# Optimization experiments

Measured on AMD Instinct MI355X. Metric: run time of the kernel, lower is better.

Reference implementation:

```python
import jax, jax.numpy as jnp
import numpy as np

HEADS = 8
DIM_HEAD = 64
EPS = 1e-5  # fp32 eps in ChanLayerNorm


def chan_layer_norm(x, g):
    # x: [b, c, h, w]; normalize over channel dim with biased variance
    mean = jnp.mean(x, axis=1, keepdims=True)
    var = jnp.var(x, axis=1, keepdims=True)
    return (x - mean) * jax.lax.rsqrt(var + EPS) * g[None, :, None, None]


def setup_inputs() -> dict:
    key = jax.random.key(0)
    k1, k2, k3 = jax.random.split(key, 3)
    dim, inner = 512, HEADS * DIM_HEAD
    fmap = jax.random.normal(k1, (16, dim, 64, 64), dtype=jnp.float32)
    # 1x1 conv weights (no bias); scaled like typical init to keep softmax unsaturated
    w_qkv = jax.random.normal(k2, (3 * inner, dim), dtype=jnp.float32) * 0.02
    w_out = jax.random.normal(k3, (dim, inner), dtype=jnp.float32) * 0.02
    g1 = jnp.ones((dim,), dtype=jnp.float32)
    g2 = jnp.ones((dim,), dtype=jnp.float32)
    return {"fmap": fmap, "g1": g1, "w_qkv": w_qkv, "w_out": w_out, "g2": g2}


def reference(fmap, g1, w_qkv, w_out, g2):
    b, c, X, Y = fmap.shape
    h, dh = HEADS, DIM_HEAD
    n = X * Y  # seq_len
    scale = dh ** -0.5

    x = chan_layer_norm(fmap, g1)
    # 1x1 conv == channel matmul: [b, 3*inner, X, Y]
    qkv = jnp.einsum('bcxy,oc->boxy', x, w_qkv)
    q, k, v = jnp.split(qkv, 3, axis=1)

    def to_bhnc(t):
        # b (h c) x y -> b h n c
        return t.reshape(b, h, dh, n).transpose(0, 1, 3, 2)

    q, k, v = map(to_bhnc, (q, k, v))

    q = jax.nn.softmax(q, axis=-1) * scale          # softmax over feature dim
    k = jax.nn.softmax(k, axis=2)                   # softmax over seq dim
    v = v / jnp.linalg.norm(v, axis=-1, keepdims=True)  # l2norm
    inv_sqrt_n = 1.0 / np.sqrt(n)
    k = k * inv_sqrt_n
    v = v * inv_sqrt_n

    context = jnp.einsum('bhnd,bhne->bhde', k, v)   # small d x e context
    out = jnp.einsum('bhnd,bhde->bhne', q, context)  # [b, h, n, dh]

    # b h n d -> b (h d) x y
    out = out.transpose(0, 1, 3, 2).reshape(b, h * dh, X, Y)
    out = jax.nn.gelu(out, approximate=False)
    out = jnp.einsum('bcxy,oc->boxy', out, w_out)
    return chan_layer_norm(out, g2)
```

## Files before the change

### kernel.cpp

```cpp
#include <hip/hip_runtime.h>

typedef unsigned short u16;
typedef __attribute__((ext_vector_type(2))) float f32x2;
typedef __attribute__((ext_vector_type(4))) float f32x4;
typedef __attribute__((ext_vector_type(8))) short s16x8;
typedef __attribute__((ext_vector_type(8))) u16 u16x8;
typedef __attribute__((ext_vector_type(4))) u16 u16x4;

#define NB 16
#define CD 512
#define NS 4096
#define NHD 8

#define SBAR  __builtin_amdgcn_s_barrier()
#define SCHED __builtin_amdgcn_sched_barrier(0)
#define LGKM0 asm volatile("s_waitcnt lgkmcnt(0)" ::: "memory")
#define PRIO1 __builtin_amdgcn_s_setprio(1)
#define PRIO0 __builtin_amdgcn_s_setprio(0)

__device__ __forceinline__ float bf2f(u16 u){
  union { unsigned int i; float f; } z; z.i = ((unsigned int)u) << 16; return z.f;
}
__device__ __forceinline__ u16 f2bf(float f){
  union { float f; unsigned int i; } z; z.f = f;
  unsigned int i = z.i;
  return (u16)((i + 0x7fffu + ((i >> 16) & 1u)) >> 16);
}
__device__ __forceinline__ float gelu_f(float x){
  return 0.5f * x * (1.0f + erff(x * 0.70710678118654752440f));
}
__device__ __forceinline__ void gl_lds16(const u16* g, u16* l){
  __builtin_amdgcn_global_load_lds((const __attribute__((address_space(1))) void*)(g),
                                   (__attribute__((address_space(3))) void*)(l), 16, 0, 0);
}

__global__ void prep_w_k(const float* __restrict__ wqkv, const float* __restrict__ g1,
                         const float* __restrict__ wout, u16* __restrict__ w1b,
                         u16* __restrict__ w2b){
  int i = blockIdx.x * 256 + threadIdx.x;
  if (i < 1536*512) {
    w1b[i] = f2bf(wqkv[i] * g1[i & 511]);
  } else {
    int j = i - 1536*512;
    w2b[j] = f2bf(wout[j]);
  }
}

__global__ __launch_bounds__(512) void ln1t_k(const float* __restrict__ fmap,
                                              u16* __restrict__ xlnT){
  int b = blockIdx.y, n0 = blockIdx.x * 32;
  int t = threadIdx.x;
  int lane = t & 63, wv = t >> 6;
  __shared__ u16 Lb[512][40];
  __shared__ u16 Tt[64][36];
  __shared__ float red1[8][8][4], red2[8][8][4];
  __shared__ float mean_s[32], rstd_s[32];

  int ng = t & 7;
  float s1[4] = {0,0,0,0}, s2[4] = {0,0,0,0};
  const float* fb = fmap + ((size_t)b*CD)*NS + n0 + ng*4;
  #pragma unroll
  for (int it = 0; it < 8; ++it){
    int q = it*512 + t;
    int c = q >> 3;
    f32x4 v = *(const f32x4*)&fb[(size_t)c*NS];
    u16x4 pk;
    #pragma unroll
    for (int j = 0; j < 4; ++j){
      pk[j] = f2bf(v[j]);
      s1[j] += v[j]; s2[j] += v[j]*v[j];
    }
    *(u16x4*)&Lb[c][ng*4] = pk;
  }
  #pragma unroll
  for (int off = 8; off < 64; off <<= 1)
    #pragma unroll
    for (int j = 0; j < 4; ++j){
      s1[j] += __shfl_xor(s1[j], off, 64);
      s2[j] += __shfl_xor(s2[j], off, 64);
    }
  if (lane < 8){
    #pragma unroll
    for (int j = 0; j < 4; ++j){ red1[wv][lane][j] = s1[j]; red2[wv][lane][j] = s2[j]; }
  }
  __syncthreads();
  if (t < 32){
    int g = t >> 2, j = t & 3;
    float a = 0.f, bq = 0.f;
    #pragma unroll
    for (int w = 0; w < 8; ++w){ a += red1[w][g][j]; bq += red2[w][g][j]; }
    float mn = a * (1.f/512.f);
    float var = bq * (1.f/512.f) - mn*mn;
    mean_s[t] = mn; rstd_s[t] = rsqrtf(var + 1e-5f);
  }
  __syncthreads();

  for (int ct = 0; ct < 8; ++ct){
    {
      int cl = t >> 3, n4 = (t & 7) * 4;
      u16x4 xv = *(const u16x4*)&Lb[ct*64 + cl][n4];
      u16x4 pk;
      #pragma unroll
      for (int j = 0; j < 4; ++j)
        pk[j] = f2bf((bf2f(xv[j]) - mean_s[n4+j]) * rstd_s[n4+j]);
      *(u16x4*)&Tt[cl][n4] = pk;
    }
    __syncthreads();
    {
      int nr = t >> 4, c4 = t & 15;
      u16x4 w;
      #pragma unroll
      for (int j = 0; j < 4; ++j) w[j] = Tt[c4*4 + j][nr];
      *(u16x4*)&xlnT[((size_t)b*NS + n0 + nr)*CD + ct*64 + c4*4] = w;
    }
    __syncthreads();
  }
}

__global__ __launch_bounds__(512) void gemm1_k(const u16* __restrict__ A,
                                               const u16* __restrict__ Bm,
                                               u16* __restrict__ Cm){
  __shared__ u16 lds[2][4][8192];
  int bi = blockIdx.x;
  int xcd = bi & 7, r2 = bi >> 3;
  int gi = r2 / 6, yy = r2 - gi*6;
  int g  = gi*8 + xcd;
  int x  = g & 15, z = g >> 4;
  int o0 = yy*256, bn0 = x*256;
  int t = threadIdx.x;
  int lane = t & 63, wv = t >> 6;
  int wm = wv >> 2, wn = wv & 3;
  int fr = lane & 15, fg = lane >> 4;
  const u16* Ab = A + (size_t)o0*512;
  const u16* Bb = Bm + ((size_t)z*NS + bn0)*512;
  int li8 = lane >> 3, scn = lane & 7;

  f32x4 acc[8][4];
  #pragma unroll
  for (int i=0;i<8;++i)
    #pragma unroll
    for (int j=0;j<4;++j) acc[i][j] = (f32x4){0.f,0.f,0.f,0.f};
  s16x8 afr[4][2];
  s16x8 bfr[2][2][2];

  auto stH = [&](int slot, int half, int kt){
    #pragma unroll
    for (int it=0; it<2; ++it){
      int li = it*64 + wv*8 + li8;
      int q  = scn ^ (li & 7);
      int row;
      if (half < 2) row = ((li>>6)<<7) + half*64 + (li & 63);
      else          row = ((li>>5)<<6) + (half-2)*32 + (li & 31);
      const u16* G = (half < 2) ? Ab : Bb;
      gl_lds16(G + (size_t)row*512 + kt + q*8, &lds[slot][half][it*4096 + wv*512]);
    }
  };
  auto ldA = [&](int slot, int mq){
    #pragma unroll
    for (int mr=0;mr<4;++mr)
      #pragma unroll
      for (int ks=0;ks<2;++ks){
        int li = wm*64 + mr*16 + fr;
        int c8 = (ks*4+fg) ^ (li & 7);
        afr[mr][ks] = *(const s16x8*)&lds[slot][mq][li*64 + c8*8];
      }
  };
  auto ldB = [&](int slot, int nq){
    #pragma unroll
    for (int nr=0;nr<2;++nr)
      #pragma unroll
      for (int ks=0;ks<2;++ks){
        int li = wn*32 + nr*16 + fr;
        int c8 = (ks*4+fg) ^ (li & 7);
        bfr[nq][nr][ks] = *(const s16x8*)&lds[slot][2+nq][li*64 + c8*8];
      }
  };
  auto mm = [&](int mq, int nq){
    #pragma unroll
    for (int mr=0;mr<4;++mr)
      #pragma unroll
      for (int nr=0;nr<2;++nr)
        #pragma unroll
        for (int ks=0;ks<2;++ks)
          acc[mq*4+mr][nq*2+nr] = __builtin_amdgcn_mfma_f32_16x16x32_bf16(
              afr[mr][ks], bfr[nq][nr][ks], acc[mq*4+mr][nq*2+nr], 0,0,0);
  };

  stH(0,0,0); stH(0,2,0); stH(0,3,0); stH(0,1,0);
  asm volatile("s_waitcnt vmcnt(2)" ::: "memory");
  SBAR; SCHED;

  #pragma unroll
  for (int kt=0; kt<8; ++kt){
    int slot = kt & 1, ns = slot ^ 1, kn = (kt+1)*64;
    bool F = kt < 7;
    ldA(slot,0); ldB(slot,0); ldB(slot,1);
    if (F){ stH(ns,0,kn); stH(ns,2,kn); stH(ns,3,kn); }
    PRIO1; mm(0,0); mm(0,1); PRIO0;
    if (F) asm volatile("s_waitcnt vmcnt(6)" ::: "memory");
    else   asm volatile("s_waitcnt vmcnt(0)" ::: "memory");
    SBAR; SCHED;
    ldA(slot,1);
    if (F) stH(ns,1,kn);
    PRIO1; mm(1,1); mm(1,0); PRIO0;
    if (F) asm volatile("s_waitcnt vmcnt(2)" ::: "memory");
    SBAR; SCHED;
  }

  size_t cb = (size_t)z * 1536 * NS;
  #pragma unroll
  for (int mq=0;mq<2;++mq)
    #pragma unroll
    for (int mr=0;mr<4;++mr)
      #pragma unroll
      for (int nq=0;nq<2;++nq)
        #pragma unroll
        for (int nr=0;nr<2;++nr){
          int row = o0 + wm*128 + mq*64 + mr*16 + fg*4;
          int col = bn0 + wn*64 + nq*32 + nr*16 + fr;
          #pragma unroll
          for (int r=0;r<4;++r)
            Cm[cb + (size_t)(row+r)*NS + col] = f2bf(acc[mq*4+mr][nq*2+nr][r]);
        }
}

__global__ __launch_bounds__(512, 2) void gemm2ln_k(const u16* __restrict__ A,
                                                    const u16* __restrict__ Bm,
                                                    const float* __restrict__ g2,
                                                    float* __restrict__ out){
  __shared__ u16 lds[2][20480];
  int x = blockIdx.x, z = blockIdx.y;
  int n0 = x*128;
  int t = threadIdx.x;
  int lane = t & 63, wv = t >> 6;
  int wm = wv >> 1, wn = wv & 1;
  int fr = lane & 15, fg = lane >> 4;
  const u16* Ab = A;
  const u16* Bb = Bm + ((size_t)z*NS + n0)*512;

  int l8  = lane >> 3;
  int c8d = lane & 7;

  f32x4 acc[8][4];
  #pragma unroll
  for (int i=0;i<8;++i)
    #pragma unroll
    for (int j=0;j<4;++j) acc[i][j] = (f32x4){0.f,0.f,0.f,0.f};
  s16x8 afr[4], bfr[4];

  auto stA = [&](int slot, int kt, int bt){
    int L  = bt*64 + wv*8 + l8;
    int q  = c8d ^ (l8 & 7);
    int r  = (q >> 2)*256 + L;
    int col = kt + (q & 3)*8;
    gl_lds16(Ab + (size_t)r*512 + col, &lds[slot][(bt*64 + wv*8)*64]);
  };
  auto stB = [&](int slot, int kt){
    int L  = wv*8 + l8;
    int q  = c8d ^ (l8 & 7);
    int r  = (q >> 2)*64 + L;
    int col = kt + (q & 3)*8;
    gl_lds16(Bb + (size_t)r*512 + col, &lds[slot][16384 + (wv*8)*64]);
  };
  auto ldA = [&](int slot, int h){
    #pragma unroll
    for (int mi=0;mi<4;++mi){
      int R = wm*128 + (h*4+mi)*16 + fr;
      int L = R & 255, half = R >> 8;
      int c8 = (half*4 + fg) ^ (L & 7);
      afr[mi] = *(const s16x8*)&lds[slot][L*64 + c8*8];
    }
  };
  auto ldB = [&](int slot){
    #pragma unroll
    for (int nj=0;nj<4;++nj){
      int R = wn*64 + nj*16 + fr;
      int L = R & 63, half = R >> 6;
      int c8 = (half*4 + fg) ^ (L & 7);
      bfr[nj] = *(const s16x8*)&lds[slot][16384 + L*64 + c8*8];
    }
  };
  auto mm16 = [&](int h){
    #pragma unroll
    for (int mi=0;mi<4;++mi)
      #pragma unroll
      for (int nj=0;nj<4;++nj)
        acc[h*4+mi][nj] = __builtin_amdgcn_mfma_f32_16x16x32_bf16(
            afr[mi], bfr[nj], acc[h*4+mi][nj], 0,0,0);
  };

  stA(0,0,0); stA(0,0,1); stB(0,0); stA(0,0,2); stA(0,0,3);
  asm volatile("s_waitcnt vmcnt(0)" ::: "memory");
  SBAR; SCHED;

  #pragma unroll
  for (int kt=0; kt<16; ++kt){
    int slot = kt & 1, ns = slot ^ 1, kn = (kt+1)*32;
    ldA(slot,0); ldB(slot);
    if (kt<15){
      stA(ns,kn,0); stA(ns,kn,1); stB(ns,kn); stA(ns,kn,2); stA(ns,kn,3);
    }
    PRIO1; mm16(0); PRIO0;
    ldA(slot,1);
    PRIO1; mm16(1); PRIO0;
    if (kt<15) asm volatile("s_waitcnt vmcnt(0)" ::: "memory");
    SBAR; SCHED;
  }

  __syncthreads();
  float* red1 = (float*)&lds[0][0];
  float* red2 = red1 + 512;
  float* ms   = red2 + 512;
  float* rs   = ms + 128;
  float s1[4], s2[4];
  #pragma unroll
  for (int nj=0;nj<4;++nj){
    float a = 0.f, b2 = 0.f;
    #pragma unroll
    for (int mi=0;mi<8;++mi)
      #pragma unroll
      for (int r=0;r<4;++r){ float v = acc[mi][nj][r]; a += v; b2 += v*v; }
    s1[nj] = a; s2[nj] = b2;
  }
  #pragma unroll
  for (int off=16; off<64; off<<=1)
    #pragma unroll
    for (int nj=0;nj<4;++nj){
      s1[nj] += __shfl_xor(s1[nj], off, 64);
      s2[nj] += __shfl_xor(s2[nj], off, 64);
    }
  if (fg == 0){
    #pragma unroll
    for (int nj=0;nj<4;++nj){
      int c = wn*64 + nj*16 + fr;
      red1[wm*128 + c] = s1[nj];
      red2[wm*128 + c] = s2[nj];
    }
  }
  __syncthreads();
  if (t < 128){
    float a  = red1[t] + red1[128+t] + red1[256+t] + red1[384+t];
    float b2 = red2[t] + red2[128+t] + red2[256+t] + red2[384+t];
    float mn = a * (1.f/512.f);
    float var = b2 * (1.f/512.f) - mn*mn;
    ms[t] = mn; rs[t] = rsqrtf(var + 1e-5f);
  }
  __syncthreads();
  float mc[4], rc[4];
  #pragma unroll
  for (int nj=0;nj<4;++nj){
    int c = wn*64 + nj*16 + fr;
    mc[nj] = ms[c]; rc[nj] = rs[c];
  }
  float* ob = out + (size_t)z*CD*NS + n0;
  #pragma unroll
  for (int mi=0;mi<8;++mi)
    #pragma unroll
    for (int r=0;r<4;++r){
      int row = wm*128 + mi*16 + fg*4 + r;
      float gg = g2[row];
      #pragma unroll
      for (int nj=0;nj<4;++nj)
        ob[(size_t)row*NS + wn*64 + nj*16 + fr] = (acc[mi][nj][r] - mc[nj])*rc[nj]*gg;
    }
}

__global__ __launch_bounds__(256) void ctxpart_k(const u16* __restrict__ qkv,
                                                 float* __restrict__ part,
                                                 float* __restrict__ mS){
  int chunk = blockIdx.x, bh = blockIdx.y;
  int b = bh >> 3, h = bh & 7;
  int t = threadIdx.x;
  int lane = t & 63, wv = t >> 6;
  int fr = lane & 15, fg = lane >> 4;
  __shared__ u16 KT[64*128];
  __shared__ u16 VT[64*128];
  __shared__ float invn_s[128];
  const u16* kb = qkv + ((size_t)(b*1536 + 512  + h*64))*NS;
  const u16* vb = qkv + ((size_t)(b*1536 + 1024 + h*64))*NS;
  int d = t >> 2, q = t & 3;

  float sloc = 0.f;

  f32x4 acc[4][4];
  #pragma unroll
  for (int i=0;i<4;++i)
    #pragma unroll
    for (int j=0;j<4;++j) acc[i][j] = (f32x4){0.f,0.f,0.f,0.f};

  for (int nt = 0; nt < 4; ++nt){
    int n0 = chunk*512 + nt*128;
    if (nt) __syncthreads();
    u16x8 kreg[4];
    #pragma unroll
    for (int s = 0; s < 4; ++s){
      int c0 = q*32 + s*8;
      u16x8 vv = *(const u16x8*)&vb[(size_t)d*NS + n0 + c0];
      *(u16x8*)&VT[d*128 + (c0 ^ ((d&7)<<3))] = vv;
      kreg[s] = *(const u16x8*)&kb[(size_t)d*NS + n0 + c0];
    }
    __syncthreads();
    {
      int col = t >> 1, half = t & 1;
      float ss = 0.f;
      #pragma unroll
      for (int e2 = 0; e2 < 32; ++e2){
        int e = half*32 + e2;
        float xv = bf2f(VT[e*128 + (col ^ ((e&7)<<3))]);
        ss += xv*xv;
      }
      ss += __shfl_xor(ss, 1, 64);
      if (half == 0) invn_s[col] = rsqrtf(ss);
    }
    __syncthreads();
    #pragma unroll
    for (int s = 0; s < 4; ++s){
      int c0 = q*32 + s*8;
      u16x8 kk = kreg[s];
      u16x8 ek;
      #pragma unroll
      for (int j = 0; j < 8; ++j){
        float e = __expf(bf2f(kk[j]));
        sloc += e;
        ek[j] = f2bf(e * invn_s[c0 + j]);
      }
      *(u16x8*)&KT[d*128 + (c0 ^ ((d&7)<<3))] = ek;
    }
    __syncthreads();
    int kc = wv*32 + fg*8;
    s16x8 af[4], bfr[4];
    #pragma unroll
    for (int i=0;i<4;++i){
      int ra = i*16 + fr;
      af[i]  = *(const s16x8*)&KT[ra*128 + (kc ^ ((ra&7)<<3))];
      bfr[i] = *(const s16x8*)&VT[ra*128 + (kc ^ ((ra&7)<<3))];
    }
    #pragma unroll
    for (int i=0;i<4;++i)
      #pragma unroll
      for (int j=0;j<4;++j)
        acc[i][j] = __builtin_amdgcn_mfma_f32_16x16x32_bf16(af[i], bfr[j], acc[i][j], 0,0,0);
  }

  sloc += __shfl_xor(sloc, 1, 64);
  sloc += __shfl_xor(sloc, 2, 64);
  if (q == 0){
    size_t mb = ((size_t)bh*8 + chunk)*128;
    mS[mb + d]      = 0.0f;
    mS[mb + 64 + d] = sloc;
  }

  float* buf0 = (float*)KT;
  float* buf1 = (float*)VT;
  auto dump = [&](float* bf){
    #pragma unroll
    for (int i=0;i<4;++i)
      #pragma unroll
      for (int j=0;j<4;++j)
        #pragma unroll
        for (int r=0;r<4;++r) bf[((i*4+j)*4+r)*64 + lane] = acc[i][j][r];
  };
  auto addin = [&](float* bf){
    #pragma unroll
    for (int i=0;i<4;++i)
      #pragma unroll
      for (int j=0;j<4;++j)
        #pragma unroll
        for (int r=0;r<4;++r) acc[i][j][r] += bf[((i*4+j)*4+r)*64 + lane];
  };
  __syncthreads();
  if (wv==1) dump(buf0);
  if (wv==3) dump(buf1);
  __syncthreads();
  if (wv==0) addin(buf0);
  if (wv==2) addin(buf1);
  __syncthreads();
  if (wv==2) dump(buf0);
  __syncthreads();
  if (wv==0){
    addin(buf0);
    float* pp = part + ((size_t)bh*8 + chunk)*4096;
    #pragma unroll
    for (int i=0;i<4;++i)
      #pragma unroll
      for (int j=0;j<4;++j)
        #pragma unroll
        for (int r=0;r<4;++r)
          pp[(i*16+fg*4+r)*64 + j*16+fr] = acc[i][j][r];
  }
}

__global__ void ctxred_k(const float* __restrict__ part, const float* __restrict__ mS,
                         float* __restrict__ ctx){
  int bh = blockIdx.x, t = threadIdx.x;
  __shared__ float fs[8][64];
  if (t < 64){
    int d = t;
    float mc[8];
    float mx = -3.0e38f;
    #pragma unroll
    for (int c=0;c<8;++c){ mc[c] = mS[((size_t)bh*8 + c)*128 + d]; mx = fmaxf(mx, mc[c]); }
    float es[8]; float denom = 0.f;
    #pragma unroll
    for (int c=0;c<8;++c){
      es[c] = __expf(mc[c] - mx);
      denom += es[c] * mS[((size_t)bh*8 + c)*128 + 64 + d];
    }
    float inv = 1.0f / (denom * 4096.0f);
    #pragma unroll
    for (int c=0;c<8;++c) fs[c][d] = es[c] * inv;
  }
  __syncthreads();
  #pragma unroll
  for (int i=0;i<16;++i){
    int idx = t + i*256;
    int d = idx >> 6;
    float s = 0.f;
    #pragma unroll
    for (int ch=0; ch<8; ++ch) s += fs[ch][d] * part[((size_t)bh*8 + ch)*4096 + idx];
    ctx[(size_t)bh*4096 + idx] = s;
  }
}

__global__ __launch_bounds__(256) void attnout_k(const u16* __restrict__ qkv,
                                                 const float* __restrict__ ctx,
                                                 u16* __restrict__ gT){
  int bh = blockIdx.y;
  int b = bh >> 3, h = bh & 7;
  int n0 = blockIdx.x * 256;
  int t = threadIdx.x;
  int lane = t & 63, wv = t >> 6;
  int fr = lane & 15, fg = lane >> 4;
  __shared__ u16 P[256][72];
  __shared__ u16 cT[64][72];

  const float* cs = ctx + (size_t)bh*4096;
  #pragma unroll
  for (int i=0;i<16;++i){
    int idx = i*256 + t;
    int d = idx >> 6, e = idx & 63;
    cT[e][d] = f2bf(cs[idx]);
  }

  const u16* qb = qkv + ((size_t)(b*1536 + h*64))*NS + n0 + t;
  float p[64];
  #pragma unroll
  for (int d=0; d<64; ++d) p[d] = bf2f(qb[(size_t)d*NS]);
  float m = p[0];
  #pragma unroll
  for (int d=1; d<64; ++d) m = fmaxf(m, p[d]);
  float s = 0.f;
  #pragma unroll
  for (int d=0; d<64; ++d){ p[d] = __expf(p[d]-m); s += p[d]; }
  float inv = 0.125f / s;
  #pragma unroll
  for (int d0=0; d0<8; ++d0){
    u16x8 pk;
    #pragma unroll
    for (int j=0;j<8;++j) pk[j] = f2bf(p[d0*8+j] * inv);
    *(u16x8*)&P[t][d0*8] = pk;
  }
  __syncthreads();

  f32x4 acc[4][4];
  #pragma unroll
  for (int i=0;i<4;++i)
    #pragma unroll
    for (int j=0;j<4;++j) acc[i][j] = (f32x4){0.f,0.f,0.f,0.f};
  #pragma unroll
  for (int k=0; k<2; ++k){
    s16x8 af[4], bfr[4];
    #pragma unroll
    for (int i=0;i<4;++i){
      af[i]  = *(const s16x8*)&P[wv*64 + i*16 + fr][k*32 + fg*8];
      bfr[i] = *(const s16x8*)&cT[i*16 + fr][k*32 + fg*8];
    }
    #pragma unroll
    for (int i=0;i<4;++i)
      #pragma unroll
      for (int j=0;j<4;++j)
        acc[i][j] = __builtin_amdgcn_mfma_f32_16x16x32_bf16(af[i], bfr[j], acc[i][j], 0,0,0);
  }

  #pragma unroll
  for (int i=0;i<4;++i)
    #pragma unroll
    for (int j=0;j<4;++j)
      #pragma unroll
      for (int r=0;r<4;++r)
        P[wv*64 + i*16 + fg*4 + r][j*16 + fr] = f2bf(gelu_f(acc[i][j][r]));

  int sub = lane >> 4, e4 = (lane & 15) * 4;
  #pragma unroll
  for (int it=0; it<16; ++it){
    int row = wv*64 + it*4 + sub;
    *(u16x4*)&gT[((size_t)b*NS + n0 + row)*CD + h*64 + e4] = *(u16x4*)&P[row][e4];
  }
}

extern "C" void kernel_launch(void* const* d_in, const int* in_sizes, int n_in,
                              void* d_out, int out_size, void* d_ws, size_t ws_size,
                              hipStream_t stream) {
  const float* fmap = (const float*)d_in[0];
  const float* g1   = (const float*)d_in[1];
  const float* wqkv = (const float*)d_in[2];
  const float* wout = (const float*)d_in[3];
  const float* g2   = (const float*)d_in[4];
  float* out = (float*)d_out;

  char* ws = (char*)d_ws;
  size_t off = 0;
  auto alloc = [&](size_t bytes) -> void* {
    void* p = ws + off;
    off += (bytes + 255) & ~(size_t)255;
    return p;
  };
  u16*   qkv  = (u16*)alloc((size_t)16*1536*4096*2);
  u16*   xlnT = (u16*)alloc((size_t)16*4096*512*2);
  u16*   gT   = xlnT;
  float* part = (float*)alloc((size_t)128*8*4096*4);
  float* mS   = (float*)alloc((size_t)128*8*128*4);
  float* ctx  = (float*)alloc((size_t)128*4096*4);
  u16*   w1b  = (u16*)alloc((size_t)1536*512*2);
  u16*   w2b  = (u16*)alloc((size_t)512*512*2);
  if (off > ws_size) return;

  prep_w_k<<<4096, 256, 0, stream>>>(wqkv, g1, wout, w1b, w2b);
  ln1t_k<<<dim3(128,16), 512, 0, stream>>>(fmap, xlnT);
  gemm1_k<<<1536, 512, 0, stream>>>(w1b, xlnT, qkv);
  ctxpart_k<<<dim3(8,128), 256, 0, stream>>>(qkv, part, mS);
  ctxred_k<<<128, 256, 0, stream>>>(part, mS, ctx);
  attnout_k<<<dim3(16,128), 256, 0, stream>>>(qkv, ctx, gT);
  gemm2ln_k<<<dim3(32,16), 512, 0, stream>>>(w2b, gT, g2, out);
}
```

Measured before the change: 314.4 us.

## Fuse attention output and GELU into the output-projection GEMM

The separate attnout kernel is removed. Its work (q softmax over the feature dim, multiply by context, GELU) is now computed per head inside the gemm2 kernel, which writes the GELU tile straight into the swizzled B LDS buffer instead of making a gT round trip through global memory. This saves the bf16 gT write and re-read and one launch. In exchange the GEMM main loop now holds serial softmax and context MFMA phases, uses more LDS, and drops the occupancy hint of 2 from launch_bounds, which may lower occupancy and weaken load overlap.

New measurement: 308.9 us. About the same (-1.8%).

```diff
diff --git a/kernel.cpp b/kernel.cpp
--- a/kernel.cpp
+++ b/kernel.cpp
@@ -14,7 +14,6 @@
 
 #define SBAR  __builtin_amdgcn_s_barrier()
 #define SCHED __builtin_amdgcn_sched_barrier(0)
-#define LGKM0 asm volatile("s_waitcnt lgkmcnt(0)" ::: "memory")
 #define PRIO1 __builtin_amdgcn_s_setprio(1)
 #define PRIO0 __builtin_amdgcn_s_setprio(0)
 
@@ -224,22 +223,25 @@
         }
 }
 
-__global__ __launch_bounds__(512, 2) void gemm2ln_k(const u16* __restrict__ A,
-                                                    const u16* __restrict__ Bm,
-                                                    const float* __restrict__ g2,
-                                                    float* __restrict__ out){
-  __shared__ u16 lds[2][20480];
+__global__ __launch_bounds__(512) void gemm2f_k(const u16* __restrict__ A,
+                                                const u16* __restrict__ qkv,
+                                                const float* __restrict__ ctx,
+                                                const float* __restrict__ g2,
+                                                float* __restrict__ out){
+  __shared__ u16 Ar[2][16384];
+  __shared__ u16 Bh[2][4096];
+  __shared__ u16 P[128][72];
+  __shared__ u16 cT[64][72];
+  __shared__ float invP[128];
   int x = blockIdx.x, z = blockIdx.y;
   int n0 = x*128;
   int t = threadIdx.x;
   int lane = t & 63, wv = t >> 6;
   int wm = wv >> 1, wn = wv & 1;
+  int wn2 = wv >> 2, we = wv & 3;
   int fr = lane & 15, fg = lane >> 4;
+  int l8 = lane >> 3, c8d = lane & 7;
   const u16* Ab = A;
-  const u16* Bb = Bm + ((size_t)z*NS + n0)*512;
-
-  int l8  = lane >> 3;
-  int c8d = lane & 7;
 
   f32x4 acc[8][4];
   #pragma unroll
@@ -248,67 +250,122 @@
     for (int j=0;j<4;++j) acc[i][j] = (f32x4){0.f,0.f,0.f,0.f};
   s16x8 afr[4], bfr[4];
 
-  auto stA = [&](int slot, int kt, int bt){
-    int L  = bt*64 + wv*8 + l8;
-    int q  = c8d ^ (l8 & 7);
-    int r  = (q >> 2)*256 + L;
-    int col = kt + (q & 3)*8;
-    gl_lds16(Ab + (size_t)r*512 + col, &lds[slot][(bt*64 + wv*8)*64]);
-  };
-  auto stB = [&](int slot, int kt){
-    int L  = wv*8 + l8;
-    int q  = c8d ^ (l8 & 7);
-    int r  = (q >> 2)*64 + L;
-    int col = kt + (q & 3)*8;
-    gl_lds16(Bb + (size_t)r*512 + col, &lds[slot][16384 + (wv*8)*64]);
-  };
-  auto ldA = [&](int slot, int h){
+  auto stA4 = [&](int slot, int kt){
+    #pragma unroll
+    for (int bt=0; bt<4; ++bt){
+      int L  = bt*64 + wv*8 + l8;
+      int q  = c8d ^ (l8 & 7);
+      int r  = (q >> 2)*256 + L;
+      int col = kt + (q & 3)*8;
+      gl_lds16(Ab + (size_t)r*512 + col, &Ar[slot][(bt*64 + wv*8)*64]);
+    }
+  };
+  auto ldA = [&](int slot, int h2){
     #pragma unroll
     for (int mi=0;mi<4;++mi){
-      int R = wm*128 + (h*4+mi)*16 + fr;
+      int R = wm*128 + (h2*4+mi)*16 + fr;
       int L = R & 255, half = R >> 8;
       int c8 = (half*4 + fg) ^ (L & 7);
-      afr[mi] = *(const s16x8*)&lds[slot][L*64 + c8*8];
-    }
-  };
-  auto ldB = [&](int slot){
+      afr[mi] = *(const s16x8*)&Ar[slot][L*64 + c8*8];
+    }
+  };
+  auto ldBh = [&](int kt2){
     #pragma unroll
     for (int nj=0;nj<4;++nj){
       int R = wn*64 + nj*16 + fr;
       int L = R & 63, half = R >> 6;
       int c8 = (half*4 + fg) ^ (L & 7);
-      bfr[nj] = *(const s16x8*)&lds[slot][16384 + L*64 + c8*8];
-    }
-  };
-  auto mm16 = [&](int h){
+      bfr[nj] = *(const s16x8*)&Bh[kt2][L*64 + c8*8];
+    }
+  };
+  auto mm16 = [&](int h2){
     #pragma unroll
     for (int mi=0;mi<4;++mi)
       #pragma unroll
       for (int nj=0;nj<4;++nj)
-        acc[h*4+mi][nj] = __builtin_amdgcn_mfma_f32_16x16x32_bf16(
-            afr[mi], bfr[nj], acc[h*4+mi][nj], 0,0,0);
-  };
-
-  stA(0,0,0); stA(0,0,1); stB(0,0); stA(0,0,2); stA(0,0,3);
-  asm volatile("s_waitcnt vmcnt(0)" ::: "memory");
-  SBAR; SCHED;
-
-  #pragma unroll
-  for (int kt=0; kt<16; ++kt){
-    int slot = kt & 1, ns = slot ^ 1, kn = (kt+1)*32;
-    ldA(slot,0); ldB(slot);
-    if (kt<15){
-      stA(ns,kn,0); stA(ns,kn,1); stB(ns,kn); stA(ns,kn,2); stA(ns,kn,3);
-    }
+        acc[h2*4+mi][nj] = __builtin_amdgcn_mfma_f32_16x16x32_bf16(
+            afr[mi], bfr[nj], acc[h2*4+mi][nj], 0,0,0);
+  };
+
+  stA4(0, 0);
+
+  for (int h = 0; h < 8; ++h){
+    const float* cs = ctx + ((size_t)(z*8 + h))*4096;
+    #pragma unroll
+    for (int i=0;i<8;++i){
+      int idx = i*512 + t;
+      cT[idx & 63][idx >> 6] = f2bf(cs[idx]);
+    }
+    {
+      int nl = wv*16 + (lane & 15);
+      int dg = lane >> 4;
+      const u16* qb = qkv + ((size_t)(z*1536 + h*64 + dg*16))*NS + n0 + nl;
+      float p[16];
+      float m = -3.0e38f;
+      #pragma unroll
+      for (int j=0;j<16;++j){ p[j] = bf2f(qb[(size_t)j*NS]); m = fmaxf(m, p[j]); }
+      m = fmaxf(m, __shfl_xor(m, 16, 64));
+      m = fmaxf(m, __shfl_xor(m, 32, 64));
+      float s = 0.f;
+      #pragma unroll
+      for (int j=0;j<16;++j){ p[j] = __expf(p[j]-m); s += p[j]; }
+      s += __shfl_xor(s, 16, 64);
+      s += __shfl_xor(s, 32, 64);
+      u16x8 pk;
+      #pragma unroll
+      for (int j=0;j<8;++j) pk[j] = f2bf(p[j]);
+      *(u16x8*)&P[nl][dg*16] = pk;
+      #pragma unroll
+      for (int j=0;j<8;++j) pk[j] = f2bf(p[8+j]);
+      *(u16x8*)&P[nl][dg*16+8] = pk;
+      if (dg == 0) invP[nl] = 0.125f / s;
+    }
+    __syncthreads();
+    stA4(1, (2*h+1)*32);
+
+    f32x4 a2[4];
+    #pragma unroll
+    for (int i=0;i<4;++i) a2[i] = (f32x4){0.f,0.f,0.f,0.f};
+    #pragma unroll
+    for (int ks=0; ks<2; ++ks){
+      s16x8 bfx = *(const s16x8*)&cT[we*16 + fr][ks*32 + fg*8];
+      #pragma unroll
+      for (int nf=0; nf<4; ++nf){
+        s16x8 afx = *(const s16x8*)&P[wn2*64 + nf*16 + fr][ks*32 + fg*8];
+        a2[nf] = __builtin_amdgcn_mfma_f32_16x16x32_bf16(afx, bfx, a2[nf], 0,0,0);
+      }
+    }
+    {
+      int kt2w = we >> 1;
+      #pragma unroll
+      for (int nf=0; nf<4; ++nf)
+        #pragma unroll
+        for (int r=0; r<4; ++r){
+          int nl2 = wn2*64 + nf*16 + fg*4 + r;
+          int e = we*16 + fr;
+          int col = e & 31;
+          int L = nl2 & 63;
+          int c8 = ((nl2>>6)*4 + (col>>3)) ^ (L & 7);
+          Bh[kt2w][L*64 + c8*8 + (col&7)] = f2bf(gelu_f(a2[nf][r] * invP[nl2]));
+        }
+    }
+    asm volatile("s_waitcnt vmcnt(4)" ::: "memory");
+    __syncthreads();
+    ldA(0,0); ldBh(0);
     PRIO1; mm16(0); PRIO0;
-    ldA(slot,1);
+    ldA(0,1);
     PRIO1; mm16(1); PRIO0;
-    if (kt<15) asm volatile("s_waitcnt vmcnt(0)" ::: "memory");
-    SBAR; SCHED;
-  }
-
-  __syncthreads();
-  float* red1 = (float*)&lds[0][0];
+    asm volatile("s_waitcnt vmcnt(0)" ::: "memory");
+    __syncthreads();
+    if (h < 7) stA4(0, (2*h+2)*32);
+    ldA(1,0); ldBh(1);
+    PRIO1; mm16(0); PRIO0;
+    ldA(1,1);
+    PRIO1; mm16(1); PRIO0;
+  }
+
+  __syncthreads();
+  float* red1 = (float*)&Ar[0][0];
   float* red2 = red1 + 512;
   float* ms   = red2 + 512;
   float* rs   = ms + 128;
@@ -522,82 +579,6 @@
   }
 }
 
-__global__ __launch_bounds__(256) void attnout_k(const u16* __restrict__ qkv,
-                                                 const float* __restrict__ ctx,
-                                                 u16* __restrict__ gT){
-  int bh = blockIdx.y;
-  int b = bh >> 3, h = bh & 7;
-  int n0 = blockIdx.x * 256;
-  int t = threadIdx.x;
-  int lane = t & 63, wv = t >> 6;
-  int fr = lane & 15, fg = lane >> 4;
-  __shared__ u16 P[256][72];
-  __shared__ u16 cT[64][72];
-
-  const float* cs = ctx + (size_t)bh*4096;
-  #pragma unroll
-  for (int i=0;i<16;++i){
-    int idx = i*256 + t;
-    int d = idx >> 6, e = idx & 63;
-    cT[e][d] = f2bf(cs[idx]);
-  }
-
-  const u16* qb = qkv + ((size_t)(b*1536 + h*64))*NS + n0 + t;
-  float p[64];
-  #pragma unroll
-  for (int d=0; d<64; ++d) p[d] = bf2f(qb[(size_t)d*NS]);
-  float m = p[0];
-  #pragma unroll
-  for (int d=1; d<64; ++d) m = fmaxf(m, p[d]);
-  float s = 0.f;
-  #pragma unroll
-  for (int d=0; d<64; ++d){ p[d] = __expf(p[d]-m); s += p[d]; }
-  float inv = 0.125f / s;
-  #pragma unroll
-  for (int d0=0; d0<8; ++d0){
-    u16x8 pk;
-    #pragma unroll
-    for (int j=0;j<8;++j) pk[j] = f2bf(p[d0*8+j] * inv);
-    *(u16x8*)&P[t][d0*8] = pk;
-  }
-  __syncthreads();
-
-  f32x4 acc[4][4];
-  #pragma unroll
-  for (int i=0;i<4;++i)
-    #pragma unroll
-    for (int j=0;j<4;++j) acc[i][j] = (f32x4){0.f,0.f,0.f,0.f};
-  #pragma unroll
-  for (int k=0; k<2; ++k){
-    s16x8 af[4], bfr[4];
-    #pragma unroll
-    for (int i=0;i<4;++i){
-      af[i]  = *(const s16x8*)&P[wv*64 + i*16 + fr][k*32 + fg*8];
-      bfr[i] = *(const s16x8*)&cT[i*16 + fr][k*32 + fg*8];
-    }
-    #pragma unroll
-    for (int i=0;i<4;++i)
-      #pragma unroll
-      for (int j=0;j<4;++j)
-        acc[i][j] = __builtin_amdgcn_mfma_f32_16x16x32_bf16(af[i], bfr[j], acc[i][j], 0,0,0);
-  }
-
-  #pragma unroll
-  for (int i=0;i<4;++i)
-    #pragma unroll
-    for (int j=0;j<4;++j)
-      #pragma unroll
-      for (int r=0;r<4;++r)
-        P[wv*64 + i*16 + fg*4 + r][j*16 + fr] = f2bf(gelu_f(acc[i][j][r]));
-
-  int sub = lane >> 4, e4 = (lane & 15) * 4;
-  #pragma unroll
-  for (int it=0; it<16; ++it){
-    int row = wv*64 + it*4 + sub;
-    *(u16x4*)&gT[((size_t)b*NS + n0 + row)*CD + h*64 + e4] = *(u16x4*)&P[row][e4];
-  }
-}
-
 extern "C" void kernel_launch(void* const* d_in, const int* in_sizes, int n_in,
                               void* d_out, int out_size, void* d_ws, size_t ws_size,
                               hipStream_t stream) {
@@ -617,7 +598,6 @@
   };
   u16*   qkv  = (u16*)alloc((size_t)16*1536*4096*2);
   u16*   xlnT = (u16*)alloc((size_t)16*4096*512*2);
-  u16*   gT   = xlnT;
   float* part = (float*)alloc((size_t)128*8*4096*4);
   float* mS   = (float*)alloc((size_t)128*8*128*4);
   float* ctx  = (float*)alloc((size_t)128*4096*4);
@@ -630,6 +610,5 @@
   gemm1_k<<<1536, 512, 0, stream>>>(w1b, xlnT, qkv);
   ctxpart_k<<<dim3(8,128), 256, 0, stream>>>(qkv, part, mS);
   ctxred_k<<<128, 256, 0, stream>>>(part, mS, ctx);
-  attnout_k<<<dim3(16,128), 256, 0, stream>>>(qkv, ctx, gT);
-  gemm2ln_k<<<dim3(32,16), 512, 0, stream>>>(w2b, gT, g2, out);
-}
+  gemm2f_k<<<dim3(32,16), 512, 0, stream>>>(w2b, qkv, ctx, g2, out);
+}
```
